# Kernel tuning notes

Measured on AMD Instinct MI355X. Metric: run time of the kernel, lower is better.

## Reference

```python
import jax, jax.numpy as jnp
import numpy as np

B, T, N, IN, H, K = 8, 10, 50, 6, 256, 4
E = N * (N - 1)


def setup_inputs() -> dict:
    key = jax.random.key(0)
    ks = jax.random.split(key, 22)
    p = lambda k, shape: jax.random.normal(k, shape, jnp.float32) * 0.05
    return {
        "inputs": jax.random.normal(ks[0], (B, T, N, IN), jnp.float32),
        "sampled_edges": jax.random.uniform(ks[1], (B, T, E, K), dtype=jnp.float32),
        "msg_w1": p(ks[2], (K, H, 2 * H)), "msg_b1": p(ks[3], (K, H)),
        "msg_w2": p(ks[4], (K, H, H)), "msg_b2": p(ks[5], (K, H)),
        "w_hr": p(ks[6], (H, H)), "w_hi": p(ks[7], (H, H)), "w_hh": p(ks[8], (H, H)),
        "w_ir": p(ks[9], (H, IN)), "b_ir": p(ks[10], (H,)),
        "w_ii": p(ks[11], (H, IN)), "b_ii": p(ks[12], (H,)),
        "w_in": p(ks[13], (H, IN)), "b_in": p(ks[14], (H,)),
        "w_o1": p(ks[15], (H, H)), "b_o1": p(ks[16], (H,)),
        "w_o2": p(ks[17], (H, H)), "b_o2": p(ks[18], (H,)),
        "w_o3": p(ks[19], (IN, H)), "b_o3": p(ks[20], (IN,)),
    }


def reference(inputs, sampled_edges, msg_w1, msg_b1, msg_w2, msg_b2,
              w_hr, w_hi, w_hh, w_ir, b_ir, w_ii, b_ii, w_in, b_in,
              w_o1, b_o1, w_o2, b_o2, w_o3, b_o3):
    b, t, n, _ = inputs.shape
    k = msg_w1.shape[0]
    h = msg_w1.shape[1]
    # fully-connected directed graph, no self loops (static indices)
    send_np, recv_np = np.where(np.ones((n, n)) - np.eye(n))
    send = jnp.asarray(send_np)
    recv = jnp.asarray(recv_np)
    norm = float(k) - 1.0  # skip_first_edge_type = True

    def single_step(ins, rel, hidden):
        # ins: [B,N,IN], rel: [B,E,K], hidden: [B,N,H]
        pre = jnp.concatenate([hidden[:, recv], hidden[:, send]], axis=-1)  # [B,E,2H]
        all_msgs = jnp.zeros((b, pre.shape[1], h), inputs.dtype)
        for i in range(1, k):  # skip first edge type
            m = jnp.tanh(jnp.einsum('bef,hf->beh', pre, msg_w1[i]) + msg_b1[i])
            m = jnp.tanh(jnp.einsum('beh,jh->bej', m, msg_w2[i]) + msg_b2[i])
            all_msgs = all_msgs + m * rel[:, :, i:i + 1] / norm
        # scatter-add messages to receiver nodes (replaces onehot matmul)
        agg = jnp.zeros((b, n, h), inputs.dtype).at[:, recv].add(all_msgs) / (n - 1)
        r = jax.nn.sigmoid(ins @ w_ir.T + b_ir + agg @ w_hr.T)
        ig = jax.nn.sigmoid(ins @ w_ii.T + b_ii + agg @ w_hi.T)
        nn_ = jnp.tanh(ins @ w_in.T + b_in + r * (agg @ w_hh.T))
        hidden = (1 - ig) * nn_ + ig * hidden
        pred = jax.nn.relu(hidden @ w_o1.T + b_o1)
        pred = jax.nn.relu(pred @ w_o2.T + b_o2)
        pred = ins + (pred @ w_o3.T + b_o3)
        return pred, hidden

    x_t = jnp.swapaxes(inputs, 0, 1)         # [T,B,N,IN]
    e_t = jnp.swapaxes(sampled_edges, 0, 1)  # [T,B,E,K]
    h0 = jnp.zeros((b, n, h), inputs.dtype)

    def step(carry, xs):
        hidden, prev = carry
        xt, et, s = xs
        ins = jnp.where(s == 0, xt, prev)  # teacher_forcing=False: only step 0 uses inputs
        pred, hidden = single_step(ins, et, hidden)
        return (hidden, pred), pred

    _, preds = jax.lax.scan(step, (h0, jnp.zeros_like(x_t[0])), (x_t, e_t, jnp.arange(t)))
    return jnp.swapaxes(preds, 0, 1)  # [B,T,N,IN]
```

## Files before the change

### kernel.cpp

```cpp
#include <hip/hip_runtime.h>
#include <hip/hip_bf16.h>
#include <stdint.h>

#define B_ 8
#define T_ 10
#define N_ 50
#define IN_ 6
#define H_ 256
#define K_ 4
#define E_ 2450
#define ROWS 400
#define AP 102400

typedef __attribute__((ext_vector_type(8))) __bf16 bf16x8;
typedef __attribute__((ext_vector_type(4))) float f32x4;

__device__ __forceinline__ unsigned short f2bf(float x) {
    unsigned int u = __float_as_uint(x);
    u = (u + 0x7fffu + ((u >> 16) & 1u)) >> 16;
    return (unsigned short)u;
}
__device__ __forceinline__ unsigned pk2(float a, float b) {
    return (unsigned)f2bf(a) | ((unsigned)f2bf(b) << 16);
}
__device__ __forceinline__ float rcp_fast(float x) { return __builtin_amdgcn_rcpf(x); }
__device__ __forceinline__ float tanh_fast(float x) {
    float e = __expf(2.0f * x);
    return 1.0f - 2.0f * rcp_fast(e + 1.0f);
}
__device__ __forceinline__ float sigmoid_fast(float x) {
    return rcp_fast(1.0f + __expf(-x));
}

__global__ __launch_bounds__(256) void swizzle_weights(
        const float* __restrict__ w1, const float* __restrict__ w2,
        const float* __restrict__ whr, const float* __restrict__ whi,
        const float* __restrict__ whh, const float* __restrict__ wo1,
        const float* __restrict__ wo2,
        unsigned short* __restrict__ w1s, unsigned short* __restrict__ w2s,
        unsigned short* __restrict__ gws, unsigned short* __restrict__ wos,
        unsigned int* __restrict__ zero_region) {
    const int W1N = 3 * 16 * 16 * 64 * 8;
    const int W2N = 3 * 16 * 8 * 64 * 8;
    const int GWN = 3 * 65536;
    const int WON = 2 * 65536;
    int idx = blockIdx.x * 256 + threadIdx.x;
    if (idx < W1N) {
        int j = idx & 7, L = (idx >> 3) & 63, kt = (idx >> 9) & 15;
        int nt = (idx >> 13) & 15, i = idx >> 17;
        int n = nt * 16 + (L & 15);
        int k = kt * 32 + ((L >> 4) << 3) + j;
        w1s[idx] = f2bf(w1[((size_t)(i + 1) * H_ + n) * (2 * H_) + k]);
    } else if (idx < W1N + W2N) {
        int t = idx - W1N;
        int j = t & 7, L = (t >> 3) & 63, kt = (t >> 9) & 7;
        int nt = (t >> 12) & 15, i = t >> 16;
        int n = nt * 16 + (L & 15);
        int k = kt * 32 + ((L >> 4) << 3) + j;
        w2s[t] = f2bf(w2[((size_t)(i + 1) * H_ + n) * H_ + k]);
    } else if (idx < W1N + W2N + GWN) {
        int t = idx - (W1N + W2N);
        int j = t & 7, L = (t >> 3) & 63, kt = (t >> 9) & 7;
        int nt = (t >> 12) & 15, mat = t >> 16;
        int n = nt * 16 + (L & 15);
        int k = kt * 32 + ((L >> 4) << 3) + j;
        const float* src = (mat == 0) ? whr : (mat == 1) ? whi : whh;
        gws[t] = f2bf(src[(size_t)n * H_ + k]);
    } else if (idx < W1N + W2N + GWN + WON) {
        int t = idx - (W1N + W2N + GWN);
        int j = t & 7, L = (t >> 3) & 63, kt = (t >> 9) & 7;
        int nt = (t >> 12) & 15, g = t >> 16;
        int n = nt * 16 + (L & 15);
        int k = kt * 32 + ((L >> 4) << 3) + j;
        const float* src = (g == 0) ? wo1 : wo2;
        wos[t] = f2bf(src[(size_t)n * H_ + k]);
    } else {
        int t = idx - (W1N + W2N + GWN + WON);
        if (t < 153600) zero_region[t] = 0u;
    }
}

__global__ __launch_bounds__(512) void uv_kernel(
        const unsigned short* __restrict__ hb, const unsigned short* __restrict__ w1s,
        const float* __restrict__ b1, float* __restrict__ UV) {
    int mm = blockIdx.x / 6;
    int tyh = blockIdx.x % 6;
    int ty = tyh >> 1, half = tyh & 1;
    int lane = threadIdx.x & 63, wid = threadIdx.x >> 6;
    int col = lane & 15, q = lane >> 4;
    const bf16x8* w1f = (const bf16x8*)w1s;

    bf16x8 a[8], w[8][2];
    #pragma unroll
    for (int kt = 0; kt < 8; ++kt) {
        a[kt] = *(const bf16x8*)&hb[(size_t)(mm * 16 + col) * H_ + kt * 32 + q * 8];
        #pragma unroll
        for (int u = 0; u < 2; ++u)
            w[kt][u] = w1f[(size_t)((ty * 16 + wid * 2 + u) * 16 + half * 8 + kt) * 64 + lane];
    }
    f32x4 acc[2];
    #pragma unroll
    for (int u = 0; u < 2; ++u) acc[u] = (f32x4){0.f, 0.f, 0.f, 0.f};
    #pragma unroll
    for (int kt = 0; kt < 8; ++kt)
        #pragma unroll
        for (int u = 0; u < 2; ++u)
            acc[u] = __builtin_amdgcn_mfma_f32_16x16x32_bf16(a[kt], w[kt][u], acc[u], 0, 0, 0);

    #pragma unroll
    for (int u = 0; u < 2; ++u) {
        int nt = wid * 2 + u;
        float bias = (half == 0) ? b1[(ty + 1) * H_ + nt * 16 + col] : 0.0f;
        #pragma unroll
        for (int r = 0; r < 4; ++r)
            UV[((size_t)(mm * 16 + q * 4 + r) * 3 + ty) * 512 + half * 256 +
               nt * 16 + col] = acc[u][r] + bias;
    }
}

__global__ __launch_bounds__(256, 4) void msgagg_kernel(
        const float* __restrict__ UV, const float* __restrict__ edges,
        const unsigned short* __restrict__ w2s,
        const float* __restrict__ b2, float* __restrict__ aggP, int t) {
    __shared__ unsigned short m1F[32 * 512];
    __shared__ float relS[64];

    int ty = blockIdx.x / 400;
    int rem = blockIdx.x - ty * 400;
    int b = rem / 50;
    int r = rem - b * 50;
    int tid = threadIdx.x;
    int lane = tid & 63, wid = tid >> 6;
    int col = lane & 15, q = lane >> 4;

    if (tid < 64) {
        float v = 0.0f;
        if (tid < 50 && tid != r) {
            int e = tid * 49 + (r > tid ? r - 1 : r);
            v = edges[(((size_t)b * T_ + t) * E_ + e) * K_ + ty + 1];
        }
        relS[tid] = v;
    }

    {
        int row = wid * 16 + col;
        int sv = row < N_ ? row : N_ - 1;
        const float* Vrow = &UV[((size_t)(b * N_ + sv) * 3 + ty) * 512 + 256 + q * 8];
        const float* Urow = &UV[((size_t)(b * N_ + r) * 3 + ty) * 512 + q * 8];
        #pragma unroll
        for (int kt = 0; kt < 8; ++kt) {
            float4 v0 = *(const float4*)(Vrow + kt * 32);
            float4 v1 = *(const float4*)(Vrow + kt * 32 + 4);
            float4 u0 = *(const float4*)(Urow + kt * 32);
            float4 u1 = *(const float4*)(Urow + kt * 32 + 4);
            float m0 = tanh_fast(u0.x + v0.x);
            float m1 = tanh_fast(u0.y + v0.y);
            float m2 = tanh_fast(u0.z + v0.z);
            float m3 = tanh_fast(u0.w + v0.w);
            float m4 = tanh_fast(u1.x + v1.x);
            float m5 = tanh_fast(u1.y + v1.y);
            float m6 = tanh_fast(u1.z + v1.z);
            float m7 = tanh_fast(u1.w + v1.w);
            uint4 pk;
            pk.x = pk2(m0, m1); pk.y = pk2(m2, m3);
            pk.z = pk2(m4, m5); pk.w = pk2(m6, m7);
            *(uint4*)&m1F[(wid * 8 + kt) * 512 + lane * 8] = pk;
        }
    }
    __syncthreads();

    const bf16x8* w2f = (const bf16x8*)w2s;
    f32x4 acc[4][4];
    #pragma unroll
    for (int mt = 0; mt < 4; ++mt)
        #pragma unroll
        for (int u = 0; u < 4; ++u) acc[mt][u] = (f32x4){0.f, 0.f, 0.f, 0.f};

    #pragma unroll
    for (int kt = 0; kt < 8; ++kt) {
        bf16x8 a0 = *(const bf16x8*)&m1F[(0 * 8 + kt) * 512 + lane * 8];
        bf16x8 a1 = *(const bf16x8*)&m1F[(1 * 8 + kt) * 512 + lane * 8];
        bf16x8 a2 = *(const bf16x8*)&m1F[(2 * 8 + kt) * 512 + lane * 8];
        bf16x8 a3 = *(const bf16x8*)&m1F[(3 * 8 + kt) * 512 + lane * 8];
        #pragma unroll
        for (int u = 0; u < 4; ++u) {
            bf16x8 w = w2f[(size_t)((ty * 16 + wid * 4 + u) * 8 + kt) * 64 + lane];
            acc[0][u] = __builtin_amdgcn_mfma_f32_16x16x32_bf16(a0, w, acc[0][u], 0, 0, 0);
            acc[1][u] = __builtin_amdgcn_mfma_f32_16x16x32_bf16(a1, w, acc[1][u], 0, 0, 0);
            acc[2][u] = __builtin_amdgcn_mfma_f32_16x16x32_bf16(a2, w, acc[2][u], 0, 0, 0);
            acc[3][u] = __builtin_amdgcn_mfma_f32_16x16x32_bf16(a3, w, acc[3][u], 0, 0, 0);
        }
    }
    #pragma unroll
    for (int u = 0; u < 4; ++u) {
        float bias = b2[(ty + 1) * H_ + (wid * 4 + u) * 16 + col];
        float sum = 0.0f;
        #pragma unroll
        for (int mt = 0; mt < 4; ++mt)
            #pragma unroll
            for (int rg = 0; rg < 4; ++rg) {
                int row = mt * 16 + q * 4 + rg;
                sum += tanh_fast(acc[mt][u][rg] + bias) * relS[row];
            }
        sum += __shfl_xor(sum, 16);
        sum += __shfl_xor(sum, 32);
        if (lane < 16)
            aggP[(size_t)ty * AP + (size_t)(b * N_ + r) * H_ +
                 (wid * 4 + u) * 16 + col] = sum * (1.0f / 147.0f);
    }
}

__global__ __launch_bounds__(512) void node_kernel(
        const float* __restrict__ inputs, const float* __restrict__ aggP,
        const unsigned short* __restrict__ gws, const unsigned short* __restrict__ wos,
        float* __restrict__ hidden, unsigned short* __restrict__ hidden_bf,
        const float* __restrict__ w_ir, const float* __restrict__ b_ir,
        const float* __restrict__ w_ii, const float* __restrict__ b_ii,
        const float* __restrict__ w_in, const float* __restrict__ b_in,
        const float* __restrict__ b_o1, const float* __restrict__ b_o2,
        const float* __restrict__ w_o3, const float* __restrict__ b_o3,
        float* __restrict__ out, int t) {
    __shared__ unsigned short aggF[8 * 512];
    __shared__ unsigned short hnF[8 * 512];
    __shared__ unsigned short p1F[8 * 512];
    __shared__ float p2L[16 * 260];
    __shared__ float insS[16 * 6];

    int mm = blockIdx.x;
    int tid = threadIdx.x;
    int lane = tid & 63, wid = tid >> 6;
    int col = lane & 15, q = lane >> 4;

    const float* src = (t == 0) ? inputs : out;
    int tt = (t == 0) ? 0 : (t - 1);

    {
        int kt = tid >> 6, L = tid & 63;
        int row = mm * 16 + (L & 15);
        int k0 = kt * 32 + ((L >> 4) << 3);
        const float* p = &aggP[(size_t)row * H_ + k0];
        float4 a0 = *(const float4*)(p);
        float4 a1 = *(const float4*)(p + 4);
        float4 b0 = *(const float4*)(p + AP);
        float4 b1v = *(const float4*)(p + AP + 4);
        float4 c0 = *(const float4*)(p + 2 * AP);
        float4 c1 = *(const float4*)(p + 2 * AP + 4);
        uint4 pk;
        pk.x = pk2(a0.x + b0.x + c0.x, a0.y + b0.y + c0.y);
        pk.y = pk2(a0.z + b0.z + c0.z, a0.w + b0.w + c0.w);
        pk.z = pk2(a1.x + b1v.x + c1.x, a1.y + b1v.y + c1.y);
        pk.w = pk2(a1.z + b1v.z + c1.z, a1.w + b1v.w + c1.w);
        *(uint4*)&aggF[(size_t)kt * 512 + L * 8] = pk;
    }
    if (tid < 96) {
        int rl = tid / 6, c = tid - rl * 6;
        int row = mm * 16 + rl;
        int b = row / 50, n = row - b * 50;
        insS[rl * 6 + c] = src[(((size_t)b * T_ + tt) * N_ + n) * IN_ + c];
    }
    __syncthreads();

    const bf16x8* gwf = (const bf16x8*)gws;
    bf16x8 af[8];
    #pragma unroll
    for (int kt = 0; kt < 8; ++kt)
        af[kt] = *(const bf16x8*)&aggF[kt * 512 + lane * 8];

    f32x4 acc[3][2];
    #pragma unroll
    for (int m = 0; m < 3; ++m)
        #pragma unroll
        for (int u = 0; u < 2; ++u) acc[m][u] = (f32x4){0.f, 0.f, 0.f, 0.f};

    bf16x8 wg[2][2][3][2];
    #pragma unroll
    for (int ki = 0; ki < 2; ++ki)
        #pragma unroll
        for (int m = 0; m < 3; ++m)
            #pragma unroll
            for (int u = 0; u < 2; ++u)
                wg[0][ki][m][u] = gwf[(size_t)((m * 16 + wid * 2 + u) * 8 + ki) * 64 + lane];
    #pragma unroll
    for (int c = 0; c < 4; ++c) {
        if (c < 3) {
            #pragma unroll
            for (int ki = 0; ki < 2; ++ki)
                #pragma unroll
                for (int m = 0; m < 3; ++m)
                    #pragma unroll
                    for (int u = 0; u < 2; ++u)
                        wg[(c + 1) & 1][ki][m][u] =
                            gwf[(size_t)((m * 16 + wid * 2 + u) * 8 + (c + 1) * 2 + ki) * 64 + lane];
        }
        #pragma unroll
        for (int ki = 0; ki < 2; ++ki)
            #pragma unroll
            for (int m = 0; m < 3; ++m)
                #pragma unroll
                for (int u = 0; u < 2; ++u)
                    acc[m][u] = __builtin_amdgcn_mfma_f32_16x16x32_bf16(
                        af[c * 2 + ki], wg[c & 1][ki][m][u], acc[m][u], 0, 0, 0);
    }

    #pragma unroll
    for (int u = 0; u < 2; ++u) {
        int h = (wid * 2 + u) * 16 + col;
        float bir = b_ir[h], bii = b_ii[h], bin_ = b_in[h];
        float wir[6], wii[6], win[6];
        #pragma unroll
        for (int c = 0; c < 6; ++c) {
            wir[c] = w_ir[h * 6 + c];
            wii[c] = w_ii[h * 6 + c];
            win[c] = w_in[h * 6 + c];
        }
        #pragma unroll
        for (int rg = 0; rg < 4; ++rg) {
            int rl = q * 4 + rg;
            int row = mm * 16 + rl;
            float xr = bir, xi = bii, xn = bin_;
            #pragma unroll
            for (int c = 0; c < 6; ++c) {
                float iv = insS[rl * 6 + c];
                xr += wir[c] * iv;
                xi += wii[c] * iv;
                xn += win[c] * iv;
            }
            float rgate = sigmoid_fast(xr + acc[0][u][rg]);
            float igate = sigmoid_fast(xi + acc[1][u][rg]);
            float nn = tanh_fast(xn + rgate * acc[2][u][rg]);
            size_t off = (size_t)row * H_ + h;
            float hold = hidden[off];
            float hnew = (1.0f - igate) * nn + igate * hold;
            hidden[off] = hnew;
            hidden_bf[off] = f2bf(hnew);
            hnF[(h >> 5) * 512 + (((h >> 3) & 3) * 16 + rl) * 8 + (h & 7)] = f2bf(hnew);
        }
    }
    __syncthreads();

    const bf16x8* wof = (const bf16x8*)wos;
    {
        bf16x8 a1f[8], w1r[8][2];
        #pragma unroll
        for (int kt = 0; kt < 8; ++kt) {
            a1f[kt] = *(const bf16x8*)&hnF[kt * 512 + lane * 8];
            #pragma unroll
            for (int u = 0; u < 2; ++u)
                w1r[kt][u] = wof[(size_t)((wid * 2 + u) * 8 + kt) * 64 + lane];
        }
        f32x4 a1v[2];
        #pragma unroll
        for (int u = 0; u < 2; ++u) a1v[u] = (f32x4){0.f, 0.f, 0.f, 0.f};
        #pragma unroll
        for (int kt = 0; kt < 8; ++kt)
            #pragma unroll
            for (int u = 0; u < 2; ++u)
                a1v[u] = __builtin_amdgcn_mfma_f32_16x16x32_bf16(a1f[kt], w1r[kt][u], a1v[u], 0, 0, 0);
        #pragma unroll
        for (int u = 0; u < 2; ++u) {
            int h = (wid * 2 + u) * 16 + col;
            float bo = b_o1[h];
            #pragma unroll
            for (int rg = 0; rg < 4; ++rg) {
                int rl = q * 4 + rg;
                float v = fmaxf(a1v[u][rg] + bo, 0.0f);
                p1F[(h >> 5) * 512 + (((h >> 3) & 3) * 16 + rl) * 8 + (h & 7)] = f2bf(v);
            }
        }
    }
    __syncthreads();

    {
        bf16x8 a2f[8], w2r[8][2];
        #pragma unroll
        for (int kt = 0; kt < 8; ++kt) {
            a2f[kt] = *(const bf16x8*)&p1F[kt * 512 + lane * 8];
            #pragma unroll
            for (int u = 0; u < 2; ++u)
                w2r[kt][u] = wof[(size_t)((16 + wid * 2 + u) * 8 + kt) * 64 + lane];
        }
        f32x4 a2v[2];
        #pragma unroll
        for (int u = 0; u < 2; ++u) a2v[u] = (f32x4){0.f, 0.f, 0.f, 0.f};
        #pragma unroll
        for (int kt = 0; kt < 8; ++kt)
            #pragma unroll
            for (int u = 0; u < 2; ++u)
                a2v[u] = __builtin_amdgcn_mfma_f32_16x16x32_bf16(a2f[kt], w2r[kt][u], a2v[u], 0, 0, 0);
        #pragma unroll
        for (int u = 0; u < 2; ++u) {
            int h = (wid * 2 + u) * 16 + col;
            float bo = b_o2[h];
            #pragma unroll
            for (int rg = 0; rg < 4; ++rg) {
                int rl = q * 4 + rg;
                p2L[rl * 260 + h] = fmaxf(a2v[u][rg] + bo, 0.0f);
            }
        }
    }
    __syncthreads();

    if (tid < 192) {
        int o = tid >> 3;
        int part = tid & 7;
        #pragma unroll
        for (int pass = 0; pass < 4; ++pass) {
            int oo = o + pass * 24;
            int rl = oo / 6, c = oo - rl * 6;
            float acc3 = (part == 0) ? b_o3[c] : 0.0f;
            const float* wrow = &w_o3[c * 256];
            const float* prow = &p2L[rl * 260];
            #pragma unroll
            for (int i = 0; i < 8; ++i) {
                int k = i * 32 + part * 4;
                float4 w = *(const float4*)&wrow[k];
                float4 p = *(const float4*)&prow[k];
                acc3 += w.x * p.x + w.y * p.y + w.z * p.z + w.w * p.w;
            }
            acc3 += __shfl_xor(acc3, 1);
            acc3 += __shfl_xor(acc3, 2);
            acc3 += __shfl_xor(acc3, 4);
            if (part == 0) {
                int row = mm * 16 + rl;
                int b = row / 50, n = row - b * 50;
                out[(((size_t)b * T_ + t) * N_ + n) * IN_ + c] = insS[rl * 6 + c] + acc3;
            }
        }
    }
}

extern "C" void kernel_launch(void* const* d_in, const int* in_sizes, int n_in,
                              void* d_out, int out_size, void* d_ws, size_t ws_size,
                              hipStream_t stream) {
    const float* inputs = (const float*)d_in[0];
    const float* edges  = (const float*)d_in[1];
    const float* msg_w1 = (const float*)d_in[2];
    const float* msg_b1 = (const float*)d_in[3];
    const float* msg_w2 = (const float*)d_in[4];
    const float* msg_b2 = (const float*)d_in[5];
    const float* w_hr = (const float*)d_in[6];
    const float* w_hi = (const float*)d_in[7];
    const float* w_hh = (const float*)d_in[8];
    const float* w_ir = (const float*)d_in[9];
    const float* b_ir = (const float*)d_in[10];
    const float* w_ii = (const float*)d_in[11];
    const float* b_ii = (const float*)d_in[12];
    const float* w_in = (const float*)d_in[13];
    const float* b_in = (const float*)d_in[14];
    const float* w_o1 = (const float*)d_in[15];
    const float* b_o1 = (const float*)d_in[16];
    const float* w_o2 = (const float*)d_in[17];
    const float* b_o2 = (const float*)d_in[18];
    const float* w_o3 = (const float*)d_in[19];
    const float* b_o3 = (const float*)d_in[20];
    float* out = (float*)d_out;

    char* ws = (char*)d_ws;
    float* hidden            = (float*)(ws);
    unsigned short* hidden_bf= (unsigned short*)(ws + 409600);
    float* UV                = (float*)(ws + 614400);
    float* aggP              = (float*)(ws + 3072000);
    unsigned short* w1s      = (unsigned short*)(ws + 4300800);
    unsigned short* w2s      = (unsigned short*)(ws + 5087232);
    unsigned short* gws      = (unsigned short*)(ws + 5480448);
    unsigned short* wos      = (unsigned short*)(ws + 5873664);

    swizzle_weights<<<dim3(4184), dim3(256), 0, stream>>>(
        msg_w1, msg_w2, w_hr, w_hi, w_hh, w_o1, w_o2, w1s, w2s, gws, wos,
        (unsigned int*)ws);

    for (int t = 0; t < T_; ++t) {
        uv_kernel<<<dim3(150), dim3(512), 0, stream>>>(hidden_bf, w1s, msg_b1, UV);
        msgagg_kernel<<<dim3(1200), dim3(256), 0, stream>>>(
            UV, edges, w2s, msg_b2, aggP, t);
        node_kernel<<<dim3(25), dim3(512), 0, stream>>>(
            inputs, aggP, gws, wos, hidden, hidden_bf,
            w_ir, b_ir, w_ii, b_ii, w_in, b_in, b_o1, b_o2, w_o3, b_o3, out, t);
    }
}
```

Baseline: 538.3 us.

## Fuse UV projection into node kernel via redundant GRU recompute and ping-pong hidden

Drops the separate uv_kernel launch per timestep. The node kernel grid grows to 175 blocks: role-0 blocks run the GRU and output MLP, while six extra roles each recompute the GRU hidden update for their 16 rows and then compute one slice of the next step's UV projection straight from shared memory. Hidden state is double-buffered so the redundant readers never race with the writer. The initial UV for zero hidden is set to the bias in the setup kernel. This removes one launch and a global round trip of hidden_bf per step, at the cost of repeating the GRU gate GEMMs six extra times.

Result: faster. 494.1 us (-8.2%).

```diff
diff --git a/kernel.cpp b/kernel.cpp
--- a/kernel.cpp
+++ b/kernel.cpp
@@ -36,14 +36,15 @@
         const float* __restrict__ w1, const float* __restrict__ w2,
         const float* __restrict__ whr, const float* __restrict__ whi,
         const float* __restrict__ whh, const float* __restrict__ wo1,
-        const float* __restrict__ wo2,
+        const float* __restrict__ wo2, const float* __restrict__ b1,
         unsigned short* __restrict__ w1s, unsigned short* __restrict__ w2s,
         unsigned short* __restrict__ gws, unsigned short* __restrict__ wos,
-        unsigned int* __restrict__ zero_region) {
+        unsigned int* __restrict__ hidden_zero, float* __restrict__ UV) {
     const int W1N = 3 * 16 * 16 * 64 * 8;
     const int W2N = 3 * 16 * 8 * 64 * 8;
     const int GWN = 3 * 65536;
     const int WON = 2 * 65536;
+    const int ZN  = 102400;
     int idx = blockIdx.x * 256 + threadIdx.x;
     if (idx < W1N) {
         int j = idx & 7, L = (idx >> 3) & 63, kt = (idx >> 9) & 15;
@@ -74,47 +75,13 @@
         int k = kt * 32 + ((L >> 4) << 3) + j;
         const float* src = (g == 0) ? wo1 : wo2;
         wos[t] = f2bf(src[(size_t)n * H_ + k]);
+    } else if (idx < W1N + W2N + GWN + WON + ZN) {
+        hidden_zero[idx - (W1N + W2N + GWN + WON)] = 0u;
     } else {
-        int t = idx - (W1N + W2N + GWN + WON);
-        if (t < 153600) zero_region[t] = 0u;
-    }
-}
-
-__global__ __launch_bounds__(512) void uv_kernel(
-        const unsigned short* __restrict__ hb, const unsigned short* __restrict__ w1s,
-        const float* __restrict__ b1, float* __restrict__ UV) {
-    int mm = blockIdx.x / 6;
-    int tyh = blockIdx.x % 6;
-    int ty = tyh >> 1, half = tyh & 1;
-    int lane = threadIdx.x & 63, wid = threadIdx.x >> 6;
-    int col = lane & 15, q = lane >> 4;
-    const bf16x8* w1f = (const bf16x8*)w1s;
-
-    bf16x8 a[8], w[8][2];
-    #pragma unroll
-    for (int kt = 0; kt < 8; ++kt) {
-        a[kt] = *(const bf16x8*)&hb[(size_t)(mm * 16 + col) * H_ + kt * 32 + q * 8];
-        #pragma unroll
-        for (int u = 0; u < 2; ++u)
-            w[kt][u] = w1f[(size_t)((ty * 16 + wid * 2 + u) * 16 + half * 8 + kt) * 64 + lane];
-    }
-    f32x4 acc[2];
-    #pragma unroll
-    for (int u = 0; u < 2; ++u) acc[u] = (f32x4){0.f, 0.f, 0.f, 0.f};
-    #pragma unroll
-    for (int kt = 0; kt < 8; ++kt)
-        #pragma unroll
-        for (int u = 0; u < 2; ++u)
-            acc[u] = __builtin_amdgcn_mfma_f32_16x16x32_bf16(a[kt], w[kt][u], acc[u], 0, 0, 0);
-
-    #pragma unroll
-    for (int u = 0; u < 2; ++u) {
-        int nt = wid * 2 + u;
-        float bias = (half == 0) ? b1[(ty + 1) * H_ + nt * 16 + col] : 0.0f;
-        #pragma unroll
-        for (int r = 0; r < 4; ++r)
-            UV[((size_t)(mm * 16 + q * 4 + r) * 3 + ty) * 512 + half * 256 +
-               nt * 16 + col] = acc[u][r] + bias;
+        int t = idx - (W1N + W2N + GWN + WON + ZN);
+        int c = t & 511;
+        int ty = (t >> 9) % 3;
+        UV[t] = (c < 256) ? b1[(ty + 1) * H_ + c] : 0.0f;
     }
 }
 
@@ -210,13 +177,16 @@
     }
 }
 
-__global__ __launch_bounds__(512) void node_kernel(
+__global__ __launch_bounds__(512) void nodeuv_kernel(
         const float* __restrict__ inputs, const float* __restrict__ aggP,
         const unsigned short* __restrict__ gws, const unsigned short* __restrict__ wos,
-        float* __restrict__ hidden, unsigned short* __restrict__ hidden_bf,
+        const unsigned short* __restrict__ w1s,
+        const float* __restrict__ hid_rd, float* __restrict__ hid_wr,
+        float* __restrict__ UV,
         const float* __restrict__ w_ir, const float* __restrict__ b_ir,
         const float* __restrict__ w_ii, const float* __restrict__ b_ii,
         const float* __restrict__ w_in, const float* __restrict__ b_in,
+        const float* __restrict__ b1,
         const float* __restrict__ b_o1, const float* __restrict__ b_o2,
         const float* __restrict__ w_o3, const float* __restrict__ b_o3,
         float* __restrict__ out, int t) {
@@ -226,7 +196,10 @@
     __shared__ float p2L[16 * 260];
     __shared__ float insS[16 * 6];
 
-    int mm = blockIdx.x;
+    int role = blockIdx.x / 25;
+    int mm = blockIdx.x - role * 25;
+    if (role > 0 && t == T_ - 1) return;
+
     int tid = threadIdx.x;
     int lane = tid & 63, wid = tid >> 6;
     int col = lane & 15, q = lane >> 4;
@@ -329,14 +302,45 @@
             float igate = sigmoid_fast(xi + acc[1][u][rg]);
             float nn = tanh_fast(xn + rgate * acc[2][u][rg]);
             size_t off = (size_t)row * H_ + h;
-            float hold = hidden[off];
+            float hold = hid_rd[off];
             float hnew = (1.0f - igate) * nn + igate * hold;
-            hidden[off] = hnew;
-            hidden_bf[off] = f2bf(hnew);
+            if (role == 0) hid_wr[off] = hnew;
             hnF[(h >> 5) * 512 + (((h >> 3) & 3) * 16 + rl) * 8 + (h & 7)] = f2bf(hnew);
         }
     }
     __syncthreads();
+
+    if (role > 0) {
+        int s = role - 1;
+        int ty = s >> 1, half = s & 1;
+        const bf16x8* w1f = (const bf16x8*)w1s;
+        bf16x8 a2f[8], wv[8][2];
+        #pragma unroll
+        for (int kt = 0; kt < 8; ++kt) {
+            a2f[kt] = *(const bf16x8*)&hnF[kt * 512 + lane * 8];
+            #pragma unroll
+            for (int u = 0; u < 2; ++u)
+                wv[kt][u] = w1f[(size_t)((ty * 16 + wid * 2 + u) * 16 + half * 8 + kt) * 64 + lane];
+        }
+        f32x4 acc2[2];
+        #pragma unroll
+        for (int u = 0; u < 2; ++u) acc2[u] = (f32x4){0.f, 0.f, 0.f, 0.f};
+        #pragma unroll
+        for (int kt = 0; kt < 8; ++kt)
+            #pragma unroll
+            for (int u = 0; u < 2; ++u)
+                acc2[u] = __builtin_amdgcn_mfma_f32_16x16x32_bf16(a2f[kt], wv[kt][u], acc2[u], 0, 0, 0);
+        #pragma unroll
+        for (int u = 0; u < 2; ++u) {
+            int nt = wid * 2 + u;
+            float bias = (half == 0) ? b1[(ty + 1) * H_ + nt * 16 + col] : 0.0f;
+            #pragma unroll
+            for (int r = 0; r < 4; ++r)
+                UV[((size_t)(mm * 16 + q * 4 + r) * 3 + ty) * 512 + half * 256 +
+                   nt * 16 + col] = acc2[u][r] + bias;
+        }
+        return;
+    }
 
     const bf16x8* wof = (const bf16x8*)wos;
     {
@@ -456,25 +460,26 @@
     float* out = (float*)d_out;
 
     char* ws = (char*)d_ws;
-    float* hidden            = (float*)(ws);
-    unsigned short* hidden_bf= (unsigned short*)(ws + 409600);
-    float* UV                = (float*)(ws + 614400);
-    float* aggP              = (float*)(ws + 3072000);
-    unsigned short* w1s      = (unsigned short*)(ws + 4300800);
-    unsigned short* w2s      = (unsigned short*)(ws + 5087232);
-    unsigned short* gws      = (unsigned short*)(ws + 5480448);
-    unsigned short* wos      = (unsigned short*)(ws + 5873664);
-
-    swizzle_weights<<<dim3(4184), dim3(256), 0, stream>>>(
-        msg_w1, msg_w2, w_hr, w_hi, w_hh, w_o1, w_o2, w1s, w2s, gws, wos,
-        (unsigned int*)ws);
-
+    float* hidden0           = (float*)(ws);
+    float* hidden1           = (float*)(ws + 409600);
+    float* UV                = (float*)(ws + 819200);
+    float* aggP              = (float*)(ws + 3276800);
+    unsigned short* w1s      = (unsigned short*)(ws + 4505600);
+    unsigned short* w2s      = (unsigned short*)(ws + 5292032);
+    unsigned short* gws      = (unsigned short*)(ws + 5685248);
+    unsigned short* wos      = (unsigned short*)(ws + 6078464);
+
+    swizzle_weights<<<dim3(6384), dim3(256), 0, stream>>>(
+        msg_w1, msg_w2, w_hr, w_hi, w_hh, w_o1, w_o2, msg_b1,
+        w1s, w2s, gws, wos, (unsigned int*)hidden0, UV);
+
+    float* hid[2] = {hidden0, hidden1};
     for (int t = 0; t < T_; ++t) {
-        uv_kernel<<<dim3(150), dim3(512), 0, stream>>>(hidden_bf, w1s, msg_b1, UV);
         msgagg_kernel<<<dim3(1200), dim3(256), 0, stream>>>(
             UV, edges, w2s, msg_b2, aggP, t);
-        node_kernel<<<dim3(25), dim3(512), 0, stream>>>(
-            inputs, aggP, gws, wos, hidden, hidden_bf,
-            w_ir, b_ir, w_ii, b_ii, w_in, b_in, b_o1, b_o2, w_o3, b_o3, out, t);
-    }
-}
+        nodeuv_kernel<<<dim3(175), dim3(512), 0, stream>>>(
+            inputs, aggP, gws, wos, w1s, hid[t & 1], hid[(t + 1) & 1], UV,
+            w_ir, b_ir, w_ii, b_ii, w_in, b_in, msg_b1,
+            b_o1, b_o2, w_o3, b_o3, out, t);
+    }
+}
```
